# Kernel optimization log

Hardware: AMD Instinct MI355X
Metric: run time of the kernel (lower is better)

Reference implementation:

```python
import jax, jax.numpy as jnp
import numpy as np

B, R, C, O, I = 128, 1152, 10, 16, 338  # batch, num_routes, num_capsules, out_channels, in_channels
NUM_ITER = 3


def setup_inputs() -> dict:
    key = jax.random.key(0)
    kx, kw = jax.random.split(key)
    x = jax.random.normal(kx, (B, R, I), dtype=jnp.float32)
    W = jax.random.normal(kw, (R, C, O, I), dtype=jnp.float32)  # leading batch-1 dim of torch param dropped
    return {"x": x, "W": W}


def _squash_elementwise(s):
    # torch squash over the trailing singleton dim of s_j (B,1,C,O,1):
    # squared_norm = s**2 elementwise -> out = s*|s|/(1+s**2)
    sq = s * s
    return sq * s / ((1.0 + sq) * jnp.sqrt(sq))


def reference(x, W):
    # u_hat[b,r,c,o] = sum_i W[r,c,o,i] * x[b,r,i]
    u_hat = jnp.einsum('rcoi,bri->brco', W, x)
    b_ij = jnp.zeros((R, C), dtype=x.dtype)  # logits shared across batch
    v = None
    for it in range(NUM_ITER):
        # F.softmax(b_ij) with no dim on 4D (1,R,C,1) defaults to dim=1 -> routes axis
        c_ij = jax.nn.softmax(b_ij, axis=0)  # (R, C)
        s = jnp.einsum('rc,brco->bco', c_ij, u_hat)  # (B, C, O)
        v = _squash_elementwise(s)
        if it < NUM_ITER - 1:
            # agreement: dot over O, then mean over batch
            a = jnp.einsum('brco,bco->brc', u_hat, v).mean(axis=0)  # (R, C)
            b_ij = b_ij + a
    # torch returns v_j.squeeze(1): (B, C, O, 1)
    return v[..., None]
```

## Files before the change

### kernel.cpp

```cpp
#include <hip/hip_runtime.h>
#include <math.h>

#define B_    128
#define R_    1152
#define C_    10
#define O_    16
#define I_    338
#define CO_   160
#define SLAB  20480
#define KT    26
#define NKT   13
#define XS_STRIDE 132
#define WS_STRIDE 161
#define RS_CHUNKS 16
#define R_PER_CHUNK 72

__global__ __launch_bounds__(256) void uhat_kernel(const float* __restrict__ x,
                                                   const float* __restrict__ W,
                                                   float* __restrict__ u) {
    __shared__ float xs[KT * XS_STRIDE];
    __shared__ float wsh[KT * WS_STRIDE];
    const int r   = blockIdx.x;
    const int tid = threadIdx.x;
    const int tx  = tid & 15;
    const int ty  = tid >> 4;

    float acc[8][10];
#pragma unroll
    for (int bb = 0; bb < 8; ++bb)
#pragma unroll
        for (int cc = 0; cc < 10; ++cc) acc[bb][cc] = 0.f;

    const float* xr = x + (size_t)r * I_;
    const float* wr = W + (size_t)r * CO_ * I_;

    for (int kt = 0; kt < NKT; ++kt) {
        const int k0 = kt * KT;
#pragma unroll
        for (int it = 0; it < 13; ++it) {
            int i = tid + it * 256;
            int b = i / KT;
            int k = i - b * KT;
            xs[k * XS_STRIDE + b] = xr[(size_t)b * (R_ * I_) + k0 + k];
        }
        for (int i = tid; i < CO_ * KT; i += 256) {
            int co = i / KT;
            int k  = i - co * KT;
            wsh[k * WS_STRIDE + co] = wr[(size_t)co * I_ + k0 + k];
        }
        __syncthreads();
        for (int k = 0; k < KT; ++k) {
            float xv[8], wv[10];
#pragma unroll
            for (int bb = 0; bb < 8; ++bb) xv[bb] = xs[k * XS_STRIDE + ty * 8 + bb];
#pragma unroll
            for (int cc = 0; cc < 10; ++cc) wv[cc] = wsh[k * WS_STRIDE + cc * 16 + tx];
#pragma unroll
            for (int bb = 0; bb < 8; ++bb)
#pragma unroll
                for (int cc = 0; cc < 10; ++cc)
                    acc[bb][cc] = fmaf(xv[bb], wv[cc], acc[bb][cc]);
        }
        __syncthreads();
    }

    float* ur = u + (size_t)r * SLAB;
#pragma unroll
    for (int bb = 0; bb < 8; ++bb)
#pragma unroll
        for (int cc = 0; cc < 10; ++cc)
            ur[(ty * 8 + bb) * CO_ + cc * 16 + tx] = acc[bb][cc];
}

__global__ void softmax_kernel(const float* __restrict__ bij, float* __restrict__ cij) {
    const int c   = blockIdx.x;
    const int tid = threadIdx.x;
    __shared__ float redm[4];
    __shared__ float reds[4];
    __shared__ float bcast[2];

    float m = -1e30f;
    for (int r = tid; r < R_; r += 256) m = fmaxf(m, bij[r * C_ + c]);
#pragma unroll
    for (int off = 32; off > 0; off >>= 1) m = fmaxf(m, __shfl_down(m, off));
    if ((tid & 63) == 0) redm[tid >> 6] = m;
    __syncthreads();
    if (tid == 0) bcast[0] = fmaxf(fmaxf(redm[0], redm[1]), fmaxf(redm[2], redm[3]));
    __syncthreads();
    m = bcast[0];

    float s = 0.f;
    for (int r = tid; r < R_; r += 256) s += expf(bij[r * C_ + c] - m);
#pragma unroll
    for (int off = 32; off > 0; off >>= 1) s += __shfl_down(s, off);
    if ((tid & 63) == 0) reds[tid >> 6] = s;
    __syncthreads();
    if (tid == 0) bcast[1] = reds[0] + reds[1] + reds[2] + reds[3];
    __syncthreads();
    const float inv = 1.0f / bcast[1];
    for (int r = tid; r < R_; r += 256) cij[r * C_ + c] = expf(bij[r * C_ + c] - m) * inv;
}

__global__ void v_partial_kernel(const float* __restrict__ u, const float* __restrict__ cij,
                                 float* __restrict__ partial) {
    const int idx   = blockIdx.x * 256 + threadIdx.x;
    const int chunk = blockIdx.y;
    const int c     = (idx >> 4) % 10;
    const int r0    = chunk * R_PER_CHUNK;
    const float* up = u + (size_t)r0 * SLAB + idx;
    const float* cp = cij + r0 * C_ + c;
    float s = 0.f;
#pragma unroll 4
    for (int rr = 0; rr < R_PER_CHUNK; ++rr)
        s = fmaf(cp[rr * C_], up[(size_t)rr * SLAB], s);
    partial[chunk * SLAB + idx] = s;
}

__global__ void v_finalize_kernel(const float* __restrict__ partial, float* __restrict__ v) {
    const int idx = blockIdx.x * 256 + threadIdx.x;
    float s = 0.f;
#pragma unroll
    for (int ch = 0; ch < RS_CHUNKS; ++ch) s += partial[ch * SLAB + idx];
    v[idx] = s * fabsf(s) / (1.0f + s * s);
}

__global__ void agree_kernel(const float* __restrict__ u, const float* __restrict__ v,
                             float* __restrict__ bij) {
    const int r = blockIdx.x;
    const int l = threadIdx.x;
    const int c = threadIdx.y;
    const float* ur = u + (size_t)r * SLAB;
    float acc = 0.f;
#pragma unroll 4
    for (int k = l; k < B_ * O_; k += 64) {
        int b = k >> 4, o = k & 15;
        int off = b * CO_ + c * O_ + o;
        acc = fmaf(ur[off], v[off], acc);
    }
#pragma unroll
    for (int off = 32; off > 0; off >>= 1) acc += __shfl_down(acc, off);
    if (l == 0) bij[r * C_ + c] += acc * (1.0f / B_);
}

extern "C" void kernel_launch(void* const* d_in, const int* in_sizes, int n_in,
                              void* d_out, int out_size, void* d_ws, size_t ws_size,
                              hipStream_t stream) {
    const float* x = (const float*)d_in[0];
    const float* W = (const float*)d_in[1];
    float* out = (float*)d_out;

    float* ws      = (float*)d_ws;
    float* u       = ws;
    float* bij     = u + (size_t)R_ * SLAB;
    float* cij     = bij + R_ * C_;
    float* partial = cij + R_ * C_;
    float* v       = partial + RS_CHUNKS * SLAB;

    hipMemsetAsync(bij, 0, R_ * C_ * sizeof(float), stream);
    uhat_kernel<<<R_, 256, 0, stream>>>(x, W, u);

    for (int it = 0; it < 3; ++it) {
        softmax_kernel<<<C_, 256, 0, stream>>>(bij, cij);
        dim3 g(SLAB / 256, RS_CHUNKS);
        v_partial_kernel<<<g, 256, 0, stream>>>(u, cij, partial);
        float* vout = (it == 2) ? out : v;
        v_finalize_kernel<<<SLAB / 256, 256, 0, stream>>>(partial, vout);
        if (it < 2) agree_kernel<<<R_, dim3(64, 10), 0, stream>>>(u, v, bij);
    }
}
```

Before: 765.0 us.

## Compute u_hat with bf16x3 split MFMA instead of scalar FP32 FMAs

Rewrites the per-route u_hat GEMM so it runs on matrix cores. Each fp32 value of x and W is split into high, mid and low bf16 parts, and six bf16 MFMA products are summed to approximate fp32 accuracy. The loads into shared memory become float4 vectorised, with a zero-padded tail tile because 338 is not a multiple of 32. This replaces the scalar FMA inner loop, which was compute-bound, but adds conversion work and six times as many MFMA ops, and accuracy may be slightly lower than true fp32.

```diff
diff --git a/kernel.cpp b/kernel.cpp
--- a/kernel.cpp
+++ b/kernel.cpp
@@ -8,68 +8,166 @@
 #define I_    338
 #define CO_   160
 #define SLAB  20480
-#define KT    26
-#define NKT   13
-#define XS_STRIDE 132
-#define WS_STRIDE 161
 #define RS_CHUNKS 16
 #define R_PER_CHUNK 72
 
-__global__ __launch_bounds__(256) void uhat_kernel(const float* __restrict__ x,
-                                                   const float* __restrict__ W,
-                                                   float* __restrict__ u) {
-    __shared__ float xs[KT * XS_STRIDE];
-    __shared__ float wsh[KT * WS_STRIDE];
-    const int r   = blockIdx.x;
-    const int tid = threadIdx.x;
-    const int tx  = tid & 15;
-    const int ty  = tid >> 4;
-
-    float acc[8][10];
-#pragma unroll
-    for (int bb = 0; bb < 8; ++bb)
-#pragma unroll
-        for (int cc = 0; cc < 10; ++cc) acc[bb][cc] = 0.f;
+#define KT32   32
+#define NKT32  11
+#define TAIL   18
+#define LROW   40
+
+typedef __attribute__((ext_vector_type(8))) short bf16x8;
+typedef __attribute__((ext_vector_type(4))) float f32x4;
+
+__device__ __forceinline__ unsigned short bf16_rne(float f) {
+    unsigned int u = __float_as_uint(f);
+    return (unsigned short)((u + 0x7fffu + ((u >> 16) & 1u)) >> 16);
+}
+__device__ __forceinline__ void cvt_split3(float f, unsigned short* h,
+                                           unsigned short* m, unsigned short* l) {
+    unsigned short hb = bf16_rne(f);
+    float fh = __uint_as_float(((unsigned int)hb) << 16);
+    float r1 = f - fh;
+    unsigned short mb = bf16_rne(r1);
+    float fm = __uint_as_float(((unsigned int)mb) << 16);
+    float r2 = r1 - fm;
+    unsigned short lb = bf16_rne(r2);
+    *h = hb; *m = mb; *l = lb;
+}
+
+__global__ __launch_bounds__(256, 2) void uhat_kernel(const float* __restrict__ x,
+                                                      const float* __restrict__ W,
+                                                      float* __restrict__ u) {
+    __shared__ __align__(16) unsigned short xh[128 * LROW];
+    __shared__ __align__(16) unsigned short xm[128 * LROW];
+    __shared__ __align__(16) unsigned short xl[128 * LROW];
+    __shared__ __align__(16) unsigned short wh[160 * LROW];
+    __shared__ __align__(16) unsigned short wm[160 * LROW];
+    __shared__ __align__(16) unsigned short wl[160 * LROW];
+
+    const int r    = blockIdx.x;
+    const int tid  = threadIdx.x;
+    const int lane = tid & 63;
+    const int w    = tid >> 6;
+    const int lr   = lane & 15;
+    const int kq8  = (lane >> 4) * 8;
+
+    f32x4 acc[2][10];
+#pragma unroll
+    for (int mt = 0; mt < 2; ++mt)
+#pragma unroll
+        for (int n = 0; n < 10; ++n) acc[mt][n] = (f32x4){0.f, 0.f, 0.f, 0.f};
 
     const float* xr = x + (size_t)r * I_;
-    const float* wr = W + (size_t)r * CO_ * I_;
-
-    for (int kt = 0; kt < NKT; ++kt) {
-        const int k0 = kt * KT;
-#pragma unroll
-        for (int it = 0; it < 13; ++it) {
-            int i = tid + it * 256;
-            int b = i / KT;
-            int k = i - b * KT;
-            xs[k * XS_STRIDE + b] = xr[(size_t)b * (R_ * I_) + k0 + k];
-        }
-        for (int i = tid; i < CO_ * KT; i += 256) {
-            int co = i / KT;
-            int k  = i - co * KT;
-            wsh[k * WS_STRIDE + co] = wr[(size_t)co * I_ + k0 + k];
+    const float* wr = W + (size_t)r * (CO_ * I_);
+
+    for (int kt = 0; kt < NKT32; ++kt) {
+        const int k0 = kt * KT32;
+        if (kt != NKT32 - 1) {
+#pragma unroll
+            for (int it = 0; it < 4; ++it) {
+                int q = tid + it * 256;
+                int b = q >> 3, kq = q & 7;
+                const float* src = xr + (size_t)b * (R_ * I_) + k0 + kq * 4;
+                float4 f = *(const float4*)src;
+                ushort4 hv, mv, lv;
+                cvt_split3(f.x, &hv.x, &mv.x, &lv.x);
+                cvt_split3(f.y, &hv.y, &mv.y, &lv.y);
+                cvt_split3(f.z, &hv.z, &mv.z, &lv.z);
+                cvt_split3(f.w, &hv.w, &mv.w, &lv.w);
+                *(ushort4*)&xh[b * LROW + kq * 4] = hv;
+                *(ushort4*)&xm[b * LROW + kq * 4] = mv;
+                *(ushort4*)&xl[b * LROW + kq * 4] = lv;
+            }
+#pragma unroll
+            for (int it = 0; it < 5; ++it) {
+                int q = tid + it * 256;
+                int co = q >> 3, kq = q & 7;
+                const float* src = wr + (size_t)co * I_ + k0 + kq * 4;
+                float4 f = *(const float4*)src;
+                ushort4 hv, mv, lv;
+                cvt_split3(f.x, &hv.x, &mv.x, &lv.x);
+                cvt_split3(f.y, &hv.y, &mv.y, &lv.y);
+                cvt_split3(f.z, &hv.z, &mv.z, &lv.z);
+                cvt_split3(f.w, &hv.w, &mv.w, &lv.w);
+                *(ushort4*)&wh[co * LROW + kq * 4] = hv;
+                *(ushort4*)&wm[co * LROW + kq * 4] = mv;
+                *(ushort4*)&wl[co * LROW + kq * 4] = lv;
+            }
+        } else {
+#pragma unroll
+            for (int it = 0; it < 4; ++it) {
+                int q = tid + it * 256;
+                int b = q >> 3, kq = q & 7;
+                const float* src = xr + (size_t)b * (R_ * I_) + k0;
+                unsigned short hv[4], mv[4], lv[4];
+#pragma unroll
+                for (int j = 0; j < 4; ++j) {
+                    int kk = kq * 4 + j;
+                    float f = (kk < TAIL) ? src[kk] : 0.f;
+                    cvt_split3(f, &hv[j], &mv[j], &lv[j]);
+                }
+                *(ushort4*)&xh[b * LROW + kq * 4] = make_ushort4(hv[0], hv[1], hv[2], hv[3]);
+                *(ushort4*)&xm[b * LROW + kq * 4] = make_ushort4(mv[0], mv[1], mv[2], mv[3]);
+                *(ushort4*)&xl[b * LROW + kq * 4] = make_ushort4(lv[0], lv[1], lv[2], lv[3]);
+            }
+#pragma unroll
+            for (int it = 0; it < 5; ++it) {
+                int q = tid + it * 256;
+                int co = q >> 3, kq = q & 7;
+                const float* src = wr + (size_t)co * I_ + k0;
+                unsigned short hv[4], mv[4], lv[4];
+#pragma unroll
+                for (int j = 0; j < 4; ++j) {
+                    int kk = kq * 4 + j;
+                    float f = (kk < TAIL) ? src[kk] : 0.f;
+                    cvt_split3(f, &hv[j], &mv[j], &lv[j]);
+                }
+                *(ushort4*)&wh[co * LROW + kq * 4] = make_ushort4(hv[0], hv[1], hv[2], hv[3]);
+                *(ushort4*)&wm[co * LROW + kq * 4] = make_ushort4(mv[0], mv[1], mv[2], mv[3]);
+                *(ushort4*)&wl[co * LROW + kq * 4] = make_ushort4(lv[0], lv[1], lv[2], lv[3]);
+            }
         }
         __syncthreads();
-        for (int k = 0; k < KT; ++k) {
-            float xv[8], wv[10];
-#pragma unroll
-            for (int bb = 0; bb < 8; ++bb) xv[bb] = xs[k * XS_STRIDE + ty * 8 + bb];
-#pragma unroll
-            for (int cc = 0; cc < 10; ++cc) wv[cc] = wsh[k * WS_STRIDE + cc * 16 + tx];
-#pragma unroll
-            for (int bb = 0; bb < 8; ++bb)
-#pragma unroll
-                for (int cc = 0; cc < 10; ++cc)
-                    acc[bb][cc] = fmaf(xv[bb], wv[cc], acc[bb][cc]);
+
+        bf16x8 ah[2], am[2], al[2];
+#pragma unroll
+        for (int mt = 0; mt < 2; ++mt) {
+            int row = w * 32 + mt * 16 + lr;
+            ah[mt] = *(const bf16x8*)&xh[row * LROW + kq8];
+            am[mt] = *(const bf16x8*)&xm[row * LROW + kq8];
+            al[mt] = *(const bf16x8*)&xl[row * LROW + kq8];
+        }
+#pragma unroll
+        for (int n = 0; n < 10; ++n) {
+            int co = n * 16 + lr;
+            bf16x8 bh = *(const bf16x8*)&wh[co * LROW + kq8];
+            bf16x8 bm = *(const bf16x8*)&wm[co * LROW + kq8];
+            bf16x8 bl = *(const bf16x8*)&wl[co * LROW + kq8];
+#pragma unroll
+            for (int mt = 0; mt < 2; ++mt) {
+                acc[mt][n] = __builtin_amdgcn_mfma_f32_16x16x32_bf16(ah[mt], bh, acc[mt][n], 0, 0, 0);
+                acc[mt][n] = __builtin_amdgcn_mfma_f32_16x16x32_bf16(ah[mt], bm, acc[mt][n], 0, 0, 0);
+                acc[mt][n] = __builtin_amdgcn_mfma_f32_16x16x32_bf16(am[mt], bh, acc[mt][n], 0, 0, 0);
+                acc[mt][n] = __builtin_amdgcn_mfma_f32_16x16x32_bf16(ah[mt], bl, acc[mt][n], 0, 0, 0);
+                acc[mt][n] = __builtin_amdgcn_mfma_f32_16x16x32_bf16(am[mt], bm, acc[mt][n], 0, 0, 0);
+                acc[mt][n] = __builtin_amdgcn_mfma_f32_16x16x32_bf16(al[mt], bh, acc[mt][n], 0, 0, 0);
+            }
         }
         __syncthreads();
     }
 
     float* ur = u + (size_t)r * SLAB;
-#pragma unroll
-    for (int bb = 0; bb < 8; ++bb)
-#pragma unroll
-        for (int cc = 0; cc < 10; ++cc)
-            ur[(ty * 8 + bb) * CO_ + cc * 16 + tx] = acc[bb][cc];
+    const int rquad = (lane >> 4) * 4;
+#pragma unroll
+    for (int mt = 0; mt < 2; ++mt)
+#pragma unroll
+        for (int n = 0; n < 10; ++n)
+#pragma unroll
+            for (int reg = 0; reg < 4; ++reg) {
+                int b = w * 32 + mt * 16 + rquad + reg;
+                ur[b * CO_ + n * 16 + lr] = acc[mt][n][reg];
+            }
 }
 
 __global__ void softmax_kernel(const float* __restrict__ bij, float* __restrict__ cij) {
```

Result: faster. 637.4 us (-16.7%).
